# Optimization experiments

Hardware: AMD Instinct MI355X
Metric: run time of the kernel (lower is better)

## Reference

```python
import jax, jax.numpy as jnp
import numpy as np

B, H, S, D = 2, 8, 2048, 64

def setup_inputs() -> dict:
    key = jax.random.key(0)
    ks = jax.random.split(key, 6)
    names = ["Qx", "Kx", "Vx", "Qy", "Ky", "Vy"]
    return {n: jax.random.normal(k, (B, H, S, D), dtype=jnp.float32)
            for n, k in zip(names, ks)}

def reference(Qx, Kx, Vx, Qy, Ky, Vy):
    scale = float(np.sqrt(Qx.shape[-1]))
    # Two score matmuls: [B,H,S,S] each
    ax = jnp.einsum('bhqd,bhkd->bhqk', Qx, Kx)
    ay = jnp.einsum('bhqd,bhkd->bhqk', Qy, Ky)
    # cat(dim=1) -> reshape(B,2,H,S,S) -> mean(dim=1) == elementwise average
    attn = (ax + ay) * 0.5
    # numerically stable softmax over keys; dropout is identity in eval mode
    w = jax.nn.softmax(attn / scale, axis=-1)
    # Shared attention weights into two value matmuls
    out1 = jnp.einsum('bhqk,bhkd->bhqd', w, Vx)
    out2 = jnp.einsum('bhqk,bhkd->bhqd', w, Vy)
    return (out1, out2)
```

## Files before the change

### kernel.cpp

```cpp
#include <hip/hip_runtime.h>
#include <hip/hip_bf16.h>

typedef __attribute__((ext_vector_type(4)))  float f32x4;
typedef __attribute__((ext_vector_type(16))) float f32x16;
typedef __attribute__((ext_vector_type(8)))  short s16x8;
typedef __attribute__((ext_vector_type(4)))  short s16x4;
typedef __attribute__((ext_vector_type(4)))  int   i32x4;

#define BB 2
#define HH 8
#define SS 2048
#define DD 64
#define QBLK 64
#define KBLK 64
#define NT   (SS / KBLK)
#define NBH  (BB * HH)

#define WS_KX 0
#define WS_KY ((size_t)NBH * NT * 8192)
#define WS_VX ((size_t)2 * NBH * NT * 8192)
#define WS_VY ((size_t)3 * NBH * NT * 8192)
#define WS_NEED ((size_t)4 * NBH * NT * 8192)

__device__ __forceinline__ short f2bf(float x) {
    unsigned u = __builtin_bit_cast(unsigned, x);
    u = (u + 0x7FFFu + ((u >> 16) & 1u)) >> 16;
    return (short)u;
}

__device__ __forceinline__ unsigned cvtpk(float lo, float hi) {
    unsigned d;
    asm("v_cvt_pk_bf16_f32 %0, %1, %2" : "=v"(d) : "v"(lo), "v"(hi));
    return d;
}

__device__ __forceinline__ int swz(int row, int byteInRow) {
    return row * 128 + (byteInRow ^ ((row & 7) << 4));
}

__device__ __forceinline__ void glds16(const void* g, void* l) {
    __builtin_amdgcn_global_load_lds(
        (const __attribute__((address_space(1))) unsigned*)g,
        (__attribute__((address_space(3))) unsigned*)l, 16, 0, 0);
}

__global__ __launch_bounds__(256)
void prep_kv(const float* __restrict__ Kx, const float* __restrict__ Ky,
             const float* __restrict__ Vx, const float* __restrict__ Vy,
             char* __restrict__ ws)
{
    const int b = blockIdx.x;
    if (b < 1024) {
        const int tid  = b * 256 + threadIdx.x;
        const int dblk = tid & 7;
        const int s    = (tid >> 3) & 2047;
        const int bh   = tid >> 14;
        const size_t gi = ((size_t)bh * SS + s) * DD + dblk * 8;
        const int kt = s >> 6, row = s & 63;
        const size_t dst = (size_t)(bh * NT + kt) * 8192 + swz(row, dblk * 16);
        const float* px = Kx + gi;
        const float* py = Ky + gi;
        s16x8 a, bb;
#pragma unroll
        for (int i = 0; i < 8; ++i) { a[i] = f2bf(px[i]); bb[i] = f2bf(py[i]); }
        *(s16x8*)(ws + WS_KX + dst) = a;
        *(s16x8*)(ws + WS_KY + dst) = bb;
    } else {
        const int tid  = (b - 1024) * 256 + threadIdx.x;
        const int d    = tid & 63;
        const int sblk = (tid >> 6) & 7;
        const int kt   = (tid >> 9) & 31;
        const int bh   = tid >> 14;
        const size_t gbase = ((size_t)bh * SS + kt * 64 + sblk * 8) * DD + d;
        s16x8 a, bb;
#pragma unroll
        for (int i = 0; i < 8; ++i) {
            a[i]  = f2bf(Vx[gbase + (size_t)i * DD]);
            bb[i] = f2bf(Vy[gbase + (size_t)i * DD]);
        }
        const size_t dst = (size_t)(bh * NT + kt) * 8192 + swz(d, sblk * 16);
        *(s16x8*)(ws + WS_VX + dst) = a;
        *(s16x8*)(ws + WS_VY + dst) = bb;
    }
}

__global__ __launch_bounds__(256, 2)
void attn_main(const float* __restrict__ Qx, const float* __restrict__ Qy,
               const char* __restrict__ ws, float* __restrict__ Out)
{
    extern __shared__ char lds[];

    const int t    = threadIdx.x;
    const int lane = t & 63;
    const int w    = t >> 6;
    const int qsub = w & 1;
    const int ks   = w >> 1;
    const int l31  = lane & 31;
    const int hi   = lane >> 5;

    int bid = blockIdx.x;
    bid = (bid & 7) * 64 + (bid >> 3);
    const int bh = bid >> 5;
    const int q0 = (bid & 31) * QBLK;
    const size_t base = (size_t)bh * SS * DD;

    const int qrow = q0 + qsub * 32 + l31;
    s16x8 qbx[4], qby[4];
#pragma unroll
    for (int dc = 0; dc < 4; ++dc) {
        const int d0 = dc * 16 + hi * 8;
        const float* qp = Qx + base + (size_t)qrow * DD + d0;
        const float* qq = Qy + base + (size_t)qrow * DD + d0;
        const float4 f0 = *(const float4*)qp;
        const float4 f1 = *(const float4*)(qp + 4);
        const float4 h0 = *(const float4*)qq;
        const float4 h1 = *(const float4*)(qq + 4);
        qbx[dc][0]=f2bf(f0.x); qbx[dc][1]=f2bf(f0.y); qbx[dc][2]=f2bf(f0.z); qbx[dc][3]=f2bf(f0.w);
        qbx[dc][4]=f2bf(f1.x); qbx[dc][5]=f2bf(f1.y); qbx[dc][6]=f2bf(f1.z); qbx[dc][7]=f2bf(f1.w);
        qby[dc][0]=f2bf(h0.x); qby[dc][1]=f2bf(h0.y); qby[dc][2]=f2bf(h0.z); qby[dc][3]=f2bf(h0.w);
        qby[dc][4]=f2bf(h1.x); qby[dc][5]=f2bf(h1.y); qby[dc][6]=f2bf(h1.z); qby[dc][7]=f2bf(h1.w);
    }

    f32x16 o1_0, o1_1, o2_0, o2_1;
#pragma unroll
    for (int j = 0; j < 16; ++j) { o1_0[j] = 0.f; o1_1[j] = 0.f; o2_0[j] = 0.f; o2_1[j] = 0.f; }
    float lsum = 0.f;

    const float SCL = 0.09016844005556021f;

#define STAGE(kt_, b_)                                                             \
    do {                                                                           \
        const size_t img_ = (size_t)(bh * NT + (kt_)) * 8192 + (size_t)t * 16;     \
        char* dst_ = lds + (b_) * 32768 + t * 16;                                  \
        glds16(ws + WS_KX + img_,        dst_);                                    \
        glds16(ws + WS_KX + img_ + 4096, dst_ + 4096);                             \
        glds16(ws + WS_KY + img_,        dst_ + 8192);                             \
        glds16(ws + WS_KY + img_ + 4096, dst_ + 12288);                            \
        glds16(ws + WS_VX + img_,        dst_ + 16384);                            \
        glds16(ws + WS_VX + img_ + 4096, dst_ + 20480);                            \
        glds16(ws + WS_VY + img_,        dst_ + 24576);                            \
        glds16(ws + WS_VY + img_ + 4096, dst_ + 28672);                            \
    } while (0)

    STAGE(0, 0);
    __syncthreads();
    int cur = 0;

    for (int kt = 0; kt < NT; ++kt) {
        if (kt + 1 < NT) STAGE(kt + 1, cur ^ 1);

        const char* KxL = lds + cur * 32768;
        const char* KyL = KxL + 8192;
        const char* VxL = KxL + 16384;
        const char* VyL = KxL + 24576;

        f32x16 sc;
#pragma unroll
        for (int j = 0; j < 16; ++j) sc[j] = 0.f;
        __builtin_amdgcn_s_setprio(1);
#pragma unroll
        for (int dc = 0; dc < 4; ++dc) {
            const int off = swz(ks * 32 + l31, dc * 32 + hi * 16);
            const s16x8 ka = *(const s16x8*)(KxL + off);
            const s16x8 kb = *(const s16x8*)(KyL + off);
            sc = __builtin_amdgcn_mfma_f32_32x32x16_bf16(ka, qbx[dc], sc, 0, 0, 0);
            sc = __builtin_amdgcn_mfma_f32_32x32x16_bf16(kb, qby[dc], sc, 0, 0, 0);
        }
        __builtin_amdgcn_s_setprio(0);

        float s = 0.f;
#pragma unroll
        for (int j = 0; j < 16; ++j) {
            sc[j] = exp2f(sc[j] * SCL);
            s += sc[j];
        }
        lsum += s;

        s16x8 pa[2];
#pragma unroll
        for (int ch = 0; ch < 2; ++ch) {
            const int b8 = ch * 8;
            const unsigned x0 = cvtpk(sc[b8 + 0], sc[b8 + 1]);
            const unsigned x1 = cvtpk(sc[b8 + 2], sc[b8 + 3]);
            const unsigned y0 = cvtpk(sc[b8 + 4], sc[b8 + 5]);
            const unsigned y1 = cvtpk(sc[b8 + 6], sc[b8 + 7]);
            const unsigned xs0 = (unsigned)__shfl_xor((int)x0, 32);
            const unsigned xs1 = (unsigned)__shfl_xor((int)x1, 32);
            const unsigned ys0 = (unsigned)__shfl_xor((int)y0, 32);
            const unsigned ys1 = (unsigned)__shfl_xor((int)y1, 32);
            i32x4 pw;
            pw[0] = (int)(hi ? ys0 : x0);
            pw[1] = (int)(hi ? ys1 : x1);
            pw[2] = (int)(hi ? y0 : xs0);
            pw[3] = (int)(hi ? y1 : xs1);
            pa[ch] = __builtin_bit_cast(s16x8, pw);
        }

        __builtin_amdgcn_s_setprio(1);
#pragma unroll
        for (int ch = 0; ch < 2; ++ch) {
            const int off0 = swz(0 * 32 + l31, ks * 64 + ch * 32 + hi * 16);
            const int off1 = swz(1 * 32 + l31, ks * 64 + ch * 32 + hi * 16);
            const s16x8 vx0 = *(const s16x8*)(VxL + off0);
            const s16x8 vx1 = *(const s16x8*)(VxL + off1);
            const s16x8 vy0 = *(const s16x8*)(VyL + off0);
            const s16x8 vy1 = *(const s16x8*)(VyL + off1);
            o1_0 = __builtin_amdgcn_mfma_f32_32x32x16_bf16(pa[ch], vx0, o1_0, 0, 0, 0);
            o1_1 = __builtin_amdgcn_mfma_f32_32x32x16_bf16(pa[ch], vx1, o1_1, 0, 0, 0);
            o2_0 = __builtin_amdgcn_mfma_f32_32x32x16_bf16(pa[ch], vy0, o2_0, 0, 0, 0);
            o2_1 = __builtin_amdgcn_mfma_f32_32x32x16_bf16(pa[ch], vy1, o2_1, 0, 0, 0);
        }
        __builtin_amdgcn_s_setprio(0);

        __syncthreads();
        cur ^= 1;
    }
#undef STAGE

    const float lh = lsum + __shfl_xor(lsum, 32);

    float* ex   = (float*)lds;
    float* linv = (float*)(lds + 24576);
    const int exo = (qsub * 64 + lane) * 33;
    float* O1 = Out;
    float* O2 = Out + (size_t)BB * HH * SS * DD;

    if (ks == 1) {
#pragma unroll
        for (int j = 0; j < 16; ++j) { ex[exo + j] = o1_0[j]; ex[exo + 16 + j] = o1_1[j]; }
        ex[exo + 32] = lh;
    }
    __syncthreads();
    if (ks == 0 && hi == 0)
        linv[qsub * 32 + l31] = 1.0f / (lh + ex[exo + 32]);
    __syncthreads();
    if (ks == 0) {
#pragma unroll
        for (int j = 0; j < 16; ++j) {
            const int qr = (j & 3) + 8 * (j >> 2) + 4 * hi;
            const float invj = linv[qsub * 32 + qr];
            const size_t ob = base + (size_t)(q0 + qsub * 32 + qr) * DD + l31;
            O1[ob]      = (o1_0[j] + ex[exo + j])      * invj;
            O1[ob + 32] = (o1_1[j] + ex[exo + 16 + j]) * invj;
        }
    }
    __syncthreads();
    if (ks == 1) {
#pragma unroll
        for (int j = 0; j < 16; ++j) { ex[exo + j] = o2_0[j]; ex[exo + 16 + j] = o2_1[j]; }
    }
    __syncthreads();
    if (ks == 0) {
#pragma unroll
        for (int j = 0; j < 16; ++j) {
            const int qr = (j & 3) + 8 * (j >> 2) + 4 * hi;
            const float invj = linv[qsub * 32 + qr];
            const size_t ob = base + (size_t)(q0 + qsub * 32 + qr) * DD + l31;
            O2[ob]      = (o2_0[j] + ex[exo + j])      * invj;
            O2[ob + 32] = (o2_1[j] + ex[exo + 16 + j]) * invj;
        }
    }
}

__global__ __launch_bounds__(256, 2)
void attn_dual_fallback(const float* __restrict__ Qx, const float* __restrict__ Kx,
                        const float* __restrict__ Vx, const float* __restrict__ Qy,
                        const float* __restrict__ Ky, const float* __restrict__ Vy,
                        float* __restrict__ Out)
{
    __shared__ __attribute__((aligned(16))) char lds[40960];
    char* KxL  = lds;
    char* KyL  = lds + 8192;
    char* VtxL = lds + 16384;
    char* VtyL = lds + 24576;

    const int t    = threadIdx.x;
    const int lane = t & 63;
    const int w    = t >> 6;
    const int g    = lane >> 4;
    const int c    = lane & 15;
    char* PL = lds + 32768 + w * 2048;

    const int bid = blockIdx.x;
    const int bh  = bid >> 5;
    const int q0  = (bid & 31) * 64;
    const size_t base = (size_t)bh * SS * DD;

    const int qrowA = q0 + w * 16 + c;
    s16x8 qxf[2], qyf[2];
#pragma unroll
    for (int kk = 0; kk < 2; ++kk) {
        const int d0 = kk * 32 + g * 8;
        const float* qp = Qx + base + (size_t)qrowA * DD + d0;
        const float* qq = Qy + base + (size_t)qrowA * DD + d0;
#pragma unroll
        for (int i = 0; i < 8; ++i) { qxf[kk][i] = f2bf(qp[i]); qyf[kk][i] = f2bf(qq[i]); }
    }

    f32x4 o1[4], o2[4];
#pragma unroll
    for (int n = 0; n < 4; ++n) {
        o1[n] = (f32x4){0.f, 0.f, 0.f, 0.f};
        o2[n] = (f32x4){0.f, 0.f, 0.f, 0.f};
    }
    float m[4]    = {-1e30f, -1e30f, -1e30f, -1e30f};
    float lsum[4] = {0.f, 0.f, 0.f, 0.f};
    const float SCL = 0.09016844005556021f;

    for (int kt = 0; kt < SS / 64; ++kt) {
        __syncthreads();
#pragma unroll
        for (int j = 0; j < 4; ++j) {
            const int f   = t + 256 * j;
            const int row = f >> 4;
            const int c4  = f & 15;
            const size_t gi = base + (size_t)(kt * 64 + row) * DD + c4 * 4;
            const float4 kx = *(const float4*)(Kx + gi);
            const float4 ky = *(const float4*)(Ky + gi);
            const float4 vx = *(const float4*)(Vx + gi);
            const float4 vy = *(const float4*)(Vy + gi);
            s16x4 a; a[0]=f2bf(kx.x); a[1]=f2bf(kx.y); a[2]=f2bf(kx.z); a[3]=f2bf(kx.w);
            *(s16x4*)(KxL + swz(row, c4 * 8)) = a;
            s16x4 b; b[0]=f2bf(ky.x); b[1]=f2bf(ky.y); b[2]=f2bf(ky.z); b[3]=f2bf(ky.w);
            *(s16x4*)(KyL + swz(row, c4 * 8)) = b;
            const int d0 = c4 * 4;
            *(short*)(VtxL + swz(d0 + 0, row * 2)) = f2bf(vx.x);
            *(short*)(VtxL + swz(d0 + 1, row * 2)) = f2bf(vx.y);
            *(short*)(VtxL + swz(d0 + 2, row * 2)) = f2bf(vx.z);
            *(short*)(VtxL + swz(d0 + 3, row * 2)) = f2bf(vx.w);
            *(short*)(VtyL + swz(d0 + 0, row * 2)) = f2bf(vy.x);
            *(short*)(VtyL + swz(d0 + 1, row * 2)) = f2bf(vy.y);
            *(short*)(VtyL + swz(d0 + 2, row * 2)) = f2bf(vy.z);
            *(short*)(VtyL + swz(d0 + 3, row * 2)) = f2bf(vy.w);
        }
        __syncthreads();

        f32x4 sc[4];
#pragma unroll
        for (int n = 0; n < 4; ++n) {
            f32x4 acc = (f32x4){0.f, 0.f, 0.f, 0.f};
            const int keyrow = n * 16 + c;
#pragma unroll
            for (int kk = 0; kk < 2; ++kk) {
                const int off = swz(keyrow, (kk * 32 + g * 8) * 2);
                const s16x8 kxf = *(const s16x8*)(KxL + off);
                const s16x8 kyf = *(const s16x8*)(KyL + off);
                acc = __builtin_amdgcn_mfma_f32_16x16x32_bf16(qxf[kk], kxf, acc, 0, 0, 0);
                acc = __builtin_amdgcn_mfma_f32_16x16x32_bf16(qyf[kk], kyf, acc, 0, 0, 0);
            }
            sc[n] = acc;
        }

#pragma unroll
        for (int r = 0; r < 4; ++r) {
            float v0 = fmaxf(fmaxf(sc[0][r], sc[1][r]), fmaxf(sc[2][r], sc[3][r])) * SCL;
#pragma unroll
            for (int off = 1; off < 16; off <<= 1) v0 = fmaxf(v0, __shfl_xor(v0, off));
            const float mnew = fmaxf(m[r], v0);
            const float cr = exp2f(m[r] - mnew);
            m[r] = mnew;
            float srow = 0.f;
#pragma unroll
            for (int n = 0; n < 4; ++n) {
                const float pp = exp2f(sc[n][r] * SCL - mnew);
                srow += pp;
                *(short*)(PL + swz(g * 4 + r, (n * 16 + c) * 2)) = f2bf(pp);
            }
#pragma unroll
            for (int off = 1; off < 16; off <<= 1) srow += __shfl_xor(srow, off);
            lsum[r] = lsum[r] * cr + srow;
#pragma unroll
            for (int n = 0; n < 4; ++n) { o1[n][r] *= cr; o2[n][r] *= cr; }
        }

        s16x8 pf[2];
#pragma unroll
        for (int kk = 0; kk < 2; ++kk)
            pf[kk] = *(const s16x8*)(PL + swz(c, (kk * 32 + g * 8) * 2));
#pragma unroll
        for (int nd = 0; nd < 4; ++nd) {
            const int drow = nd * 16 + c;
#pragma unroll
            for (int kk = 0; kk < 2; ++kk) {
                const int off = swz(drow, (kk * 32 + g * 8) * 2);
                const s16x8 vxf = *(const s16x8*)(VtxL + off);
                const s16x8 vyf = *(const s16x8*)(VtyL + off);
                o1[nd] = __builtin_amdgcn_mfma_f32_16x16x32_bf16(pf[kk], vxf, o1[nd], 0, 0, 0);
                o2[nd] = __builtin_amdgcn_mfma_f32_16x16x32_bf16(pf[kk], vyf, o2[nd], 0, 0, 0);
            }
        }
    }

    float* O1 = Out;
    float* O2 = Out + (size_t)BB * HH * SS * DD;
#pragma unroll
    for (int r = 0; r < 4; ++r) {
        const float inv = 1.0f / lsum[r];
        const int qrow = q0 + w * 16 + g * 4 + r;
        const size_t ob = base + (size_t)qrow * DD + c;
#pragma unroll
        for (int nd = 0; nd < 4; ++nd) {
            O1[ob + nd * 16] = o1[nd][r] * inv;
            O2[ob + nd * 16] = o2[nd][r] * inv;
        }
    }
}

extern "C" void kernel_launch(void* const* d_in, const int* in_sizes, int n_in,
                              void* d_out, int out_size, void* d_ws, size_t ws_size,
                              hipStream_t stream) {
    const float* Qx = (const float*)d_in[0];
    const float* Kx = (const float*)d_in[1];
    const float* Vx = (const float*)d_in[2];
    const float* Qy = (const float*)d_in[3];
    const float* Ky = (const float*)d_in[4];
    const float* Vy = (const float*)d_in[5];
    float* Out = (float*)d_out;

    if (ws_size >= WS_NEED) {
        char* ws = (char*)d_ws;
        hipLaunchKernelGGL(prep_kv, dim3(2048), dim3(256), 0, stream,
                           Kx, Ky, Vx, Vy, ws);
        hipFuncSetAttribute((const void*)attn_main,
                            hipFuncAttributeMaxDynamicSharedMemorySize, 65536);
        hipLaunchKernelGGL(attn_main, dim3(NBH * (SS / QBLK)), dim3(256), 65536,
                           stream, Qx, Qy, (const char*)ws, Out);
    } else {
        hipLaunchKernelGGL(attn_dual_fallback, dim3(NBH * 32), dim3(256),
                           0, stream, Qx, Kx, Vx, Qy, Ky, Vy, Out);
    }
}
```

Baseline: 68.84 us.

## Software-pipeline softmax with next tile's QK and previous tile's PV

Restructures the key-tile loop so each iteration computes the QK scores for the current tile, reads its V fragments into registers, then runs the PV MFMAs for the previous tile before doing softmax on the current scores. A prologue handles tile 0 and an epilogue issues the final PV block. The aim is to overlap the exp/pack/shuffle softmax work with independent MFMA work instead of serializing QK, softmax and PV. In exchange it holds an extra set of V fragments and P operands in registers, raises register pressure and may lower occupancy. It also adds a barrier before the epilogue reuses LDS.

```diff
diff --git a/kernel.cpp b/kernel.cpp
--- a/kernel.cpp
+++ b/kernel.cpp
@@ -142,11 +142,93 @@
         glds16(ws + WS_VY + img_ + 4096, dst_ + 28672);                            \
     } while (0)
 
+#define QK_BLOCK(KxL_, KyL_, sc_)                                                  \
+    do {                                                                           \
+        _Pragma("unroll")                                                          \
+        for (int dc = 0; dc < 4; ++dc) {                                           \
+            const int off = swz(ks * 32 + l31, dc * 32 + hi * 16);                 \
+            const s16x8 ka = *(const s16x8*)((KxL_) + off);                        \
+            const s16x8 kb = *(const s16x8*)((KyL_) + off);                        \
+            sc_ = __builtin_amdgcn_mfma_f32_32x32x16_bf16(ka, qbx[dc], sc_, 0, 0, 0); \
+            sc_ = __builtin_amdgcn_mfma_f32_32x32x16_bf16(kb, qby[dc], sc_, 0, 0, 0); \
+        }                                                                          \
+    } while (0)
+
+#define V_READS(VxL_, VyL_, vr_)                                                   \
+    do {                                                                           \
+        _Pragma("unroll")                                                          \
+        for (int ch = 0; ch < 2; ++ch) {                                           \
+            const int off0 = swz(l31,      ks * 64 + ch * 32 + hi * 16);           \
+            const int off1 = swz(32 + l31, ks * 64 + ch * 32 + hi * 16);           \
+            vr_[ch * 4 + 0] = *(const s16x8*)((VxL_) + off0);                      \
+            vr_[ch * 4 + 1] = *(const s16x8*)((VxL_) + off1);                      \
+            vr_[ch * 4 + 2] = *(const s16x8*)((VyL_) + off0);                      \
+            vr_[ch * 4 + 3] = *(const s16x8*)((VyL_) + off1);                      \
+        }                                                                          \
+    } while (0)
+
+#define SOFTMAX_PA(sc_, pa_)                                                       \
+    do {                                                                           \
+        float s_ = 0.f;                                                            \
+        _Pragma("unroll")                                                          \
+        for (int j = 0; j < 16; ++j) { sc_[j] = exp2f(sc_[j] * SCL); s_ += sc_[j]; } \
+        lsum += s_;                                                                \
+        _Pragma("unroll")                                                          \
+        for (int ch = 0; ch < 2; ++ch) {                                           \
+            const int b8 = ch * 8;                                                 \
+            const unsigned x0 = cvtpk(sc_[b8 + 0], sc_[b8 + 1]);                   \
+            const unsigned x1 = cvtpk(sc_[b8 + 2], sc_[b8 + 3]);                   \
+            const unsigned y0 = cvtpk(sc_[b8 + 4], sc_[b8 + 5]);                   \
+            const unsigned y1 = cvtpk(sc_[b8 + 6], sc_[b8 + 7]);                   \
+            const unsigned xs0 = (unsigned)__shfl_xor((int)x0, 32);                \
+            const unsigned xs1 = (unsigned)__shfl_xor((int)x1, 32);                \
+            const unsigned ys0 = (unsigned)__shfl_xor((int)y0, 32);                \
+            const unsigned ys1 = (unsigned)__shfl_xor((int)y1, 32);                \
+            i32x4 pw;                                                              \
+            pw[0] = (int)(hi ? ys0 : x0);                                          \
+            pw[1] = (int)(hi ? ys1 : x1);                                          \
+            pw[2] = (int)(hi ? y0 : xs0);                                          \
+            pw[3] = (int)(hi ? y1 : xs1);                                          \
+            pa_[ch] = __builtin_bit_cast(s16x8, pw);                               \
+        }                                                                          \
+    } while (0)
+
+#define PV_BLOCK(pa_, vr_)                                                         \
+    do {                                                                           \
+        _Pragma("unroll")                                                          \
+        for (int ch = 0; ch < 2; ++ch) {                                           \
+            o1_0 = __builtin_amdgcn_mfma_f32_32x32x16_bf16(pa_[ch], vr_[ch*4+0], o1_0, 0, 0, 0); \
+            o1_1 = __builtin_amdgcn_mfma_f32_32x32x16_bf16(pa_[ch], vr_[ch*4+1], o1_1, 0, 0, 0); \
+            o2_0 = __builtin_amdgcn_mfma_f32_32x32x16_bf16(pa_[ch], vr_[ch*4+2], o2_0, 0, 0, 0); \
+            o2_1 = __builtin_amdgcn_mfma_f32_32x32x16_bf16(pa_[ch], vr_[ch*4+3], o2_1, 0, 0, 0); \
+        }                                                                          \
+    } while (0)
+
     STAGE(0, 0);
     __syncthreads();
-    int cur = 0;
-
-    for (int kt = 0; kt < NT; ++kt) {
+
+    s16x8 pa[2];
+    s16x8 vr[8];
+    {
+        const char* KxL = lds;
+        const char* KyL = KxL + 8192;
+        const char* VxL = KxL + 16384;
+        const char* VyL = KxL + 24576;
+        f32x16 sc;
+#pragma unroll
+        for (int j = 0; j < 16; ++j) sc[j] = 0.f;
+        __builtin_amdgcn_s_setprio(1);
+        QK_BLOCK(KxL, KyL, sc);
+        __builtin_amdgcn_s_setprio(0);
+        V_READS(VxL, VyL, vr);
+        SOFTMAX_PA(sc, pa);
+    }
+    STAGE(1, 1);
+    __syncthreads();
+    int cur = 1;
+
+#pragma unroll 2
+    for (int kt = 1; kt < NT; ++kt) {
         if (kt + 1 < NT) STAGE(kt + 1, cur ^ 1);
 
         const char* KxL = lds + cur * 32768;
@@ -157,68 +239,38 @@
         f32x16 sc;
 #pragma unroll
         for (int j = 0; j < 16; ++j) sc[j] = 0.f;
+
         __builtin_amdgcn_s_setprio(1);
-#pragma unroll
-        for (int dc = 0; dc < 4; ++dc) {
-            const int off = swz(ks * 32 + l31, dc * 32 + hi * 16);
-            const s16x8 ka = *(const s16x8*)(KxL + off);
-            const s16x8 kb = *(const s16x8*)(KyL + off);
-            sc = __builtin_amdgcn_mfma_f32_32x32x16_bf16(ka, qbx[dc], sc, 0, 0, 0);
-            sc = __builtin_amdgcn_mfma_f32_32x32x16_bf16(kb, qby[dc], sc, 0, 0, 0);
-        }
+        QK_BLOCK(KxL, KyL, sc);
+
+        s16x8 nvr[8];
+        V_READS(VxL, VyL, nvr);
+
+        PV_BLOCK(pa, vr);
+
+        SOFTMAX_PA(sc, pa);
         __builtin_amdgcn_s_setprio(0);
 
-        float s = 0.f;
-#pragma unroll
-        for (int j = 0; j < 16; ++j) {
-            sc[j] = exp2f(sc[j] * SCL);
-            s += sc[j];
-        }
-        lsum += s;
-
-        s16x8 pa[2];
-#pragma unroll
-        for (int ch = 0; ch < 2; ++ch) {
-            const int b8 = ch * 8;
-            const unsigned x0 = cvtpk(sc[b8 + 0], sc[b8 + 1]);
-            const unsigned x1 = cvtpk(sc[b8 + 2], sc[b8 + 3]);
-            const unsigned y0 = cvtpk(sc[b8 + 4], sc[b8 + 5]);
-            const unsigned y1 = cvtpk(sc[b8 + 6], sc[b8 + 7]);
-            const unsigned xs0 = (unsigned)__shfl_xor((int)x0, 32);
-            const unsigned xs1 = (unsigned)__shfl_xor((int)x1, 32);
-            const unsigned ys0 = (unsigned)__shfl_xor((int)y0, 32);
-            const unsigned ys1 = (unsigned)__shfl_xor((int)y1, 32);
-            i32x4 pw;
-            pw[0] = (int)(hi ? ys0 : x0);
-            pw[1] = (int)(hi ? ys1 : x1);
-            pw[2] = (int)(hi ? y0 : xs0);
-            pw[3] = (int)(hi ? y1 : xs1);
-            pa[ch] = __builtin_bit_cast(s16x8, pw);
-        }
-
-        __builtin_amdgcn_s_setprio(1);
-#pragma unroll
-        for (int ch = 0; ch < 2; ++ch) {
-            const int off0 = swz(0 * 32 + l31, ks * 64 + ch * 32 + hi * 16);
-            const int off1 = swz(1 * 32 + l31, ks * 64 + ch * 32 + hi * 16);
-            const s16x8 vx0 = *(const s16x8*)(VxL + off0);
-            const s16x8 vx1 = *(const s16x8*)(VxL + off1);
-            const s16x8 vy0 = *(const s16x8*)(VyL + off0);
-            const s16x8 vy1 = *(const s16x8*)(VyL + off1);
-            o1_0 = __builtin_amdgcn_mfma_f32_32x32x16_bf16(pa[ch], vx0, o1_0, 0, 0, 0);
-            o1_1 = __builtin_amdgcn_mfma_f32_32x32x16_bf16(pa[ch], vx1, o1_1, 0, 0, 0);
-            o2_0 = __builtin_amdgcn_mfma_f32_32x32x16_bf16(pa[ch], vy0, o2_0, 0, 0, 0);
-            o2_1 = __builtin_amdgcn_mfma_f32_32x32x16_bf16(pa[ch], vy1, o2_1, 0, 0, 0);
-        }
-        __builtin_amdgcn_s_setprio(0);
+#pragma unroll
+        for (int i = 0; i < 8; ++i) vr[i] = nvr[i];
 
         __syncthreads();
         cur ^= 1;
     }
+
+    __builtin_amdgcn_s_setprio(1);
+    PV_BLOCK(pa, vr);
+    __builtin_amdgcn_s_setprio(0);
+
 #undef STAGE
+#undef QK_BLOCK
+#undef V_READS
+#undef SOFTMAX_PA
+#undef PV_BLOCK
 
     const float lh = lsum + __shfl_xor(lsum, 32);
 
+    __syncthreads();
     float* ex   = (float*)lds;
     float* linv = (float*)(lds + 24576);
     const int exo = (qsub * 64 + lane) * 33;
```

New measurement: 65.85 us. 1.05x faster.
